# Performance work log

Measured on AMD Instinct MI355X. Metric: run time of the kernel, lower is better.

Reference implementation:

```python
import jax, jax.numpy as jnp
import numpy as np

B, N = 2048, 8192
K = 64          # subset size / number of relaxation steps
TAU = 1.0
EPS = 1e-10


def setup_inputs() -> dict:
    key = jax.random.key(0)
    k1, k2 = jax.random.split(key)
    scores = jax.random.normal(k1, (B, N), dtype=jnp.float32)
    # Gumbel(0,1) noise, same as torch.distributions.Gumbel(zeros, ones).sample()
    u = jax.random.uniform(k2, (B, N), dtype=jnp.float32, minval=1e-20, maxval=1.0)
    g = -jnp.log(-jnp.log(u))
    return {"scores": scores, "g": g}


def reference(scores, g):
    # Perturb scores with Gumbel noise
    s0 = scores + g  # [B, N]
    khot0 = jnp.zeros_like(s0)
    onehot0 = jnp.zeros_like(s0)

    def step(carry, _):
        s, khot, onehot_approx = carry
        khot_mask = jnp.maximum(1.0 - onehot_approx, EPS)   # suppress picked items
        s = s + jnp.log(khot_mask)
        onehot_approx = jax.nn.softmax(s / TAU, axis=1)
        return (s, khot + onehot_approx, onehot_approx), None

    (_, khot, _), _ = jax.lax.scan(step, (s0, khot0, onehot0), None, length=K)
    # hard=False -> return relaxed k-hot vector
    return khot
```

## Files before the change

kernel.cpp:

```cpp
#include <hip/hip_runtime.h>
#include <math.h>


#define BROWS 2048
#define NCOLS 8192
#define KSTEPS 64

#define THREADS 256
#define EPT (NCOLS / THREADS)
#define NWAVE (THREADS / 64)

__global__ __launch_bounds__(THREADS, 2) void gumbel_subset_kernel(
    const float* __restrict__ scores,
    const float* __restrict__ g,
    float* __restrict__ out)
{
    const int row = blockIdx.x;
    const int t = threadIdx.x;
    const float* __restrict__ srow = scores + (size_t)row * NCOLS;
    const float* __restrict__ grow = g + (size_t)row * NCOLS;
    float* __restrict__ orow = out + (size_t)row * NCOLS;

    float v[EPT];
    float kh[EPT];

    float m = -INFINITY;
#pragma unroll
    for (int c = 0; c < EPT / 4; ++c) {
        const int idx = c * (THREADS * 4) + t * 4;
        const float4 a = *reinterpret_cast<const float4*>(srow + idx);
        const float4 b = *reinterpret_cast<const float4*>(grow + idx);
        const float s0 = a.x + b.x;
        const float s1 = a.y + b.y;
        const float s2 = a.z + b.z;
        const float s3 = a.w + b.w;
        v[c * 4 + 0] = s0;
        v[c * 4 + 1] = s1;
        v[c * 4 + 2] = s2;
        v[c * 4 + 3] = s3;
        m = fmaxf(m, fmaxf(fmaxf(s0, s1), fmaxf(s2, s3)));
    }

    __shared__ float red[2][NWAVE];
    const int wave = t >> 6;
    const int lane = t & 63;

#pragma unroll
    for (int off = 32; off > 0; off >>= 1)
        m = fmaxf(m, __shfl_xor(m, off, 64));
    if (lane == 0) red[0][wave] = m;
    __syncthreads();
    m = fmaxf(fmaxf(red[0][0], red[0][1]), fmaxf(red[0][2], red[0][3]));
    __syncthreads();

    float sa = 0.0f, sb = 0.0f, sc = 0.0f, sd = 0.0f;
#pragma unroll
    for (int e = 0; e < EPT; e += 4) {
        v[e + 0] = __expf(v[e + 0] - m);
        v[e + 1] = __expf(v[e + 1] - m);
        v[e + 2] = __expf(v[e + 2] - m);
        v[e + 3] = __expf(v[e + 3] - m);
        kh[e + 0] = 0.0f; kh[e + 1] = 0.0f; kh[e + 2] = 0.0f; kh[e + 3] = 0.0f;
        sa += v[e + 0]; sb += v[e + 1]; sc += v[e + 2]; sd += v[e + 3];
    }

#pragma unroll 2
    for (int it = 0; it < KSTEPS; ++it) {
        float s = (sa + sb) + (sc + sd);
#pragma unroll
        for (int off = 32; off > 0; off >>= 1)
            s += __shfl_xor(s, off, 64);

        const int buf = it & 1;
        if (lane == 0) red[buf][wave] = s;
        __syncthreads();
        const float S = (red[buf][0] + red[buf][1]) + (red[buf][2] + red[buf][3]);
        const float rinv = __builtin_amdgcn_rcpf(S);

        sa = 0.0f; sb = 0.0f; sc = 0.0f; sd = 0.0f;
#pragma unroll
        for (int e = 0; e < EPT; e += 4) {
            const float w0 = v[e + 0] * rinv;
            const float w1 = v[e + 1] * rinv;
            const float w2 = v[e + 2] * rinv;
            const float w3 = v[e + 3] * rinv;
            kh[e + 0] += w0; kh[e + 1] += w1; kh[e + 2] += w2; kh[e + 3] += w3;
            v[e + 0] = __builtin_fmaf(-w0, v[e + 0], v[e + 0]);
            v[e + 1] = __builtin_fmaf(-w1, v[e + 1], v[e + 1]);
            v[e + 2] = __builtin_fmaf(-w2, v[e + 2], v[e + 2]);
            v[e + 3] = __builtin_fmaf(-w3, v[e + 3], v[e + 3]);
            sa += v[e + 0]; sb += v[e + 1]; sc += v[e + 2]; sd += v[e + 3];
        }
    }

#pragma unroll
    for (int c = 0; c < EPT / 4; ++c) {
        const int idx = c * (THREADS * 4) + t * 4;
        float4 o;
        o.x = kh[c * 4 + 0];
        o.y = kh[c * 4 + 1];
        o.z = kh[c * 4 + 2];
        o.w = kh[c * 4 + 3];
        *reinterpret_cast<float4*>(orow + idx) = o;
    }
}

extern "C" void kernel_launch(void* const* d_in, const int* in_sizes, int n_in,
                              void* d_out, int out_size, void* d_ws, size_t ws_size,
                              hipStream_t stream) {
    const float* scores = (const float*)d_in[0];
    const float* g = (const float*)d_in[1];
    float* out = (float*)d_out;
    (void)in_sizes; (void)n_in; (void)out_size; (void)d_ws; (void)ws_size;

    gumbel_subset_kernel<<<BROWS, THREADS, 0, stream>>>(scores, g, out);
}
```

Baseline: 109.4 us.

## Fuse two relaxation steps per block reduction using sum-of-squares identity

The kernel now runs two softmax relaxation steps per block-wide reduction. It accumulates both the sum and the sum of squares of the unnormalized weights, and derives the second step's normalizer algebraically as S - Q/S. This halves the number of cross-wave reductions and __syncthreads barriers. The wave reduction also switches from shuffle-xor to DPP row operations plus readlane, reducing two values at once. In exchange, each step adds an extra FMA per element for the squared accumulation, and the derived normalizer may lose some floating-point accuracy.

```diff
diff --git a/kernel.cpp b/kernel.cpp
--- a/kernel.cpp
+++ b/kernel.cpp
@@ -5,10 +5,43 @@
 #define BROWS 2048
 #define NCOLS 8192
 #define KSTEPS 64
+#define NSUPER (KSTEPS / 2)
 
 #define THREADS 256
 #define EPT (NCOLS / THREADS)
 #define NWAVE (THREADS / 64)
+
+__device__ __forceinline__ float2 wave_sum2_dpp(float x, float y) {
+    int tx, ty;
+    tx = __builtin_amdgcn_update_dpp(0, __builtin_bit_cast(int, x), 0x111, 0xf, 0xf, true);
+    ty = __builtin_amdgcn_update_dpp(0, __builtin_bit_cast(int, y), 0x111, 0xf, 0xf, true);
+    x += __builtin_bit_cast(float, tx);
+    y += __builtin_bit_cast(float, ty);
+    tx = __builtin_amdgcn_update_dpp(0, __builtin_bit_cast(int, x), 0x112, 0xf, 0xf, true);
+    ty = __builtin_amdgcn_update_dpp(0, __builtin_bit_cast(int, y), 0x112, 0xf, 0xf, true);
+    x += __builtin_bit_cast(float, tx);
+    y += __builtin_bit_cast(float, ty);
+    tx = __builtin_amdgcn_update_dpp(0, __builtin_bit_cast(int, x), 0x114, 0xf, 0xf, true);
+    ty = __builtin_amdgcn_update_dpp(0, __builtin_bit_cast(int, y), 0x114, 0xf, 0xf, true);
+    x += __builtin_bit_cast(float, tx);
+    y += __builtin_bit_cast(float, ty);
+    tx = __builtin_amdgcn_update_dpp(0, __builtin_bit_cast(int, x), 0x118, 0xf, 0xf, true);
+    ty = __builtin_amdgcn_update_dpp(0, __builtin_bit_cast(int, y), 0x118, 0xf, 0xf, true);
+    x += __builtin_bit_cast(float, tx);
+    y += __builtin_bit_cast(float, ty);
+    tx = __builtin_amdgcn_update_dpp(0, __builtin_bit_cast(int, x), 0x142, 0xa, 0xf, false);
+    ty = __builtin_amdgcn_update_dpp(0, __builtin_bit_cast(int, y), 0x142, 0xa, 0xf, false);
+    x += __builtin_bit_cast(float, tx);
+    y += __builtin_bit_cast(float, ty);
+    tx = __builtin_amdgcn_update_dpp(0, __builtin_bit_cast(int, x), 0x143, 0xc, 0xf, false);
+    ty = __builtin_amdgcn_update_dpp(0, __builtin_bit_cast(int, y), 0x143, 0xc, 0xf, false);
+    x += __builtin_bit_cast(float, tx);
+    y += __builtin_bit_cast(float, ty);
+    float2 r;
+    r.x = __builtin_bit_cast(float, __builtin_amdgcn_readlane(__builtin_bit_cast(int, x), 63));
+    r.y = __builtin_bit_cast(float, __builtin_amdgcn_readlane(__builtin_bit_cast(int, y), 63));
+    return r;
+}
 
 __global__ __launch_bounds__(THREADS, 2) void gumbel_subset_kernel(
     const float* __restrict__ scores,
@@ -41,19 +74,20 @@
         m = fmaxf(m, fmaxf(fmaxf(s0, s1), fmaxf(s2, s3)));
     }
 
-    __shared__ float red[2][NWAVE];
+    __shared__ float redm[NWAVE];
+    __shared__ float2 red[2][NWAVE];
     const int wave = t >> 6;
     const int lane = t & 63;
 
 #pragma unroll
     for (int off = 32; off > 0; off >>= 1)
         m = fmaxf(m, __shfl_xor(m, off, 64));
-    if (lane == 0) red[0][wave] = m;
+    if (lane == 0) redm[wave] = m;
     __syncthreads();
-    m = fmaxf(fmaxf(red[0][0], red[0][1]), fmaxf(red[0][2], red[0][3]));
-    __syncthreads();
+    m = fmaxf(fmaxf(redm[0], redm[1]), fmaxf(redm[2], redm[3]));
 
     float sa = 0.0f, sb = 0.0f, sc = 0.0f, sd = 0.0f;
+    float qa = 0.0f, qb = 0.0f, qc = 0.0f, qd = 0.0f;
 #pragma unroll
     for (int e = 0; e < EPT; e += 4) {
         v[e + 0] = __expf(v[e + 0] - m);
@@ -62,34 +96,57 @@
         v[e + 3] = __expf(v[e + 3] - m);
         kh[e + 0] = 0.0f; kh[e + 1] = 0.0f; kh[e + 2] = 0.0f; kh[e + 3] = 0.0f;
         sa += v[e + 0]; sb += v[e + 1]; sc += v[e + 2]; sd += v[e + 3];
+        qa = __builtin_fmaf(v[e + 0], v[e + 0], qa);
+        qb = __builtin_fmaf(v[e + 1], v[e + 1], qb);
+        qc = __builtin_fmaf(v[e + 2], v[e + 2], qc);
+        qd = __builtin_fmaf(v[e + 3], v[e + 3], qd);
     }
+    __syncthreads();
 
-#pragma unroll 2
-    for (int it = 0; it < KSTEPS; ++it) {
-        float s = (sa + sb) + (sc + sd);
-#pragma unroll
-        for (int off = 32; off > 0; off >>= 1)
-            s += __shfl_xor(s, off, 64);
+    for (int k = 0; k < NSUPER; ++k) {
+        const float2 p = wave_sum2_dpp((sa + sb) + (sc + sd),
+                                       (qa + qb) + (qc + qd));
 
-        const int buf = it & 1;
-        if (lane == 0) red[buf][wave] = s;
+        const int buf = k & 1;
+        if (lane == 0) red[buf][wave] = p;
         __syncthreads();
-        const float S = (red[buf][0] + red[buf][1]) + (red[buf][2] + red[buf][3]);
-        const float rinv = __builtin_amdgcn_rcpf(S);
+        const float2 r0 = red[buf][0];
+        const float2 r1 = red[buf][1];
+        const float2 r2 = red[buf][2];
+        const float2 r3 = red[buf][3];
+        const float S1 = (r0.x + r1.x) + (r2.x + r3.x);
+        const float Q1 = (r0.y + r1.y) + (r2.y + r3.y);
+        const float ri1 = __builtin_amdgcn_rcpf(S1);
+        const float S2 = __builtin_fmaf(-Q1, ri1, S1);
+        const float ri2 = __builtin_amdgcn_rcpf(S2);
 
         sa = 0.0f; sb = 0.0f; sc = 0.0f; sd = 0.0f;
+        qa = 0.0f; qb = 0.0f; qc = 0.0f; qd = 0.0f;
 #pragma unroll
         for (int e = 0; e < EPT; e += 4) {
-            const float w0 = v[e + 0] * rinv;
-            const float w1 = v[e + 1] * rinv;
-            const float w2 = v[e + 2] * rinv;
-            const float w3 = v[e + 3] * rinv;
-            kh[e + 0] += w0; kh[e + 1] += w1; kh[e + 2] += w2; kh[e + 3] += w3;
-            v[e + 0] = __builtin_fmaf(-w0, v[e + 0], v[e + 0]);
-            v[e + 1] = __builtin_fmaf(-w1, v[e + 1], v[e + 1]);
-            v[e + 2] = __builtin_fmaf(-w2, v[e + 2], v[e + 2]);
-            v[e + 3] = __builtin_fmaf(-w3, v[e + 3], v[e + 3]);
+            const float wA0 = v[e + 0] * ri1;
+            const float wA1 = v[e + 1] * ri1;
+            const float wA2 = v[e + 2] * ri1;
+            const float wA3 = v[e + 3] * ri1;
+            kh[e + 0] += wA0; kh[e + 1] += wA1; kh[e + 2] += wA2; kh[e + 3] += wA3;
+            v[e + 0] = __builtin_fmaf(-wA0, v[e + 0], v[e + 0]);
+            v[e + 1] = __builtin_fmaf(-wA1, v[e + 1], v[e + 1]);
+            v[e + 2] = __builtin_fmaf(-wA2, v[e + 2], v[e + 2]);
+            v[e + 3] = __builtin_fmaf(-wA3, v[e + 3], v[e + 3]);
+            const float wB0 = v[e + 0] * ri2;
+            const float wB1 = v[e + 1] * ri2;
+            const float wB2 = v[e + 2] * ri2;
+            const float wB3 = v[e + 3] * ri2;
+            kh[e + 0] += wB0; kh[e + 1] += wB1; kh[e + 2] += wB2; kh[e + 3] += wB3;
+            v[e + 0] = __builtin_fmaf(-wB0, v[e + 0], v[e + 0]);
+            v[e + 1] = __builtin_fmaf(-wB1, v[e + 1], v[e + 1]);
+            v[e + 2] = __builtin_fmaf(-wB2, v[e + 2], v[e + 2]);
+            v[e + 3] = __builtin_fmaf(-wB3, v[e + 3], v[e + 3]);
             sa += v[e + 0]; sb += v[e + 1]; sc += v[e + 2]; sd += v[e + 3];
+            qa = __builtin_fmaf(v[e + 0], v[e + 0], qa);
+            qb = __builtin_fmaf(v[e + 1], v[e + 1], qb);
+            qc = __builtin_fmaf(v[e + 2], v[e + 2], qc);
+            qd = __builtin_fmaf(v[e + 3], v[e + 3], qd);
         }
     }
 
```

Result: faster. 102.0 us (-6.7%).
